# Performance work log

Hardware: AMD Instinct MI355X
Metric: run time of the kernel (lower is better)

The kernel has to match this reference:

```python
import jax, jax.numpy as jnp
import numpy as np

DIM_Q, DIM_K, HEADS = 256, 32, 4
SCALE = (DIM_Q // HEADS) ** (-0.5)


def setup_inputs() -> dict:
    key = jax.random.key(0)
    ks = jax.random.split(key, 12)
    B, C, H, W, D = 2, DIM_Q, 16, 16, 16
    inp = {
        'F_VNet': jax.random.normal(ks[0], (B, C, H, W, D), dtype=jnp.float32),
        'F_Knowledge': jax.random.normal(ks[1], (B, DIM_K, H, W, D), dtype=jnp.float32),
        # torch nn.Linear: y = x @ W.T + b, W: [out, in]
        'Wq': jax.random.normal(ks[2], (DIM_Q, DIM_Q), dtype=jnp.float32) * (DIM_Q ** -0.5),
        'bq': jnp.zeros((DIM_Q,), dtype=jnp.float32),
        'Wk': jax.random.normal(ks[3], (DIM_Q, DIM_K), dtype=jnp.float32) * (DIM_K ** -0.5),
        'bk': jnp.zeros((DIM_Q,), dtype=jnp.float32),
        'Wv': jax.random.normal(ks[4], (DIM_Q, DIM_K), dtype=jnp.float32) * (DIM_K ** -0.5),
        'bv': jnp.zeros((DIM_Q,), dtype=jnp.float32),
        'Wo': jax.random.normal(ks[5], (DIM_Q, DIM_Q), dtype=jnp.float32) * (DIM_Q ** -0.5),
        'bo': jnp.zeros((DIM_Q,), dtype=jnp.float32),
    }
    return inp


def reference(F_VNet, F_Knowledge, Wq, bq, Wk, bk, Wv, bv, Wo, bo):
    B, C, H, W, D = F_VNet.shape
    Ck = F_Knowledge.shape[1]
    # flatten spatial dims to tokens: [B, N, C]
    xq = F_VNet.reshape(B, C, -1).transpose(0, 2, 1)          # [B, Nq, dim_q]
    xk = F_Knowledge.reshape(B, Ck, -1).transpose(0, 2, 1)    # [B, Nk, dim_k]
    Q = xq @ Wq.T + bq                                        # [B, Nq, dim_q]
    K = xk @ Wk.T + bk                                        # [B, Nk, dim_q]
    V = xk @ Wv.T + bv                                        # [B, Nk, dim_q]
    attn = jax.nn.softmax(jnp.einsum('bqc,bkc->bqk', Q, K) * SCALE, axis=-1)
    out = jnp.einsum('bqk,bkc->bqc', attn, V)                 # [B, Nq, dim_q]
    out = out @ Wo.T + bo
    out = out.transpose(0, 2, 1).reshape(B, C, H, W, D)
    return F_VNet + out
```

## Files before the change

### kernel.cpp

```cpp
#include <hip/hip_runtime.h>
#include <hip/hip_bf16.h>
#include <cstdint>
#include <cstddef>

#define N_TOK 4096
#define CQ    256
#define CK    32
#define QK_SCALE 0.18033688011112042f

typedef __attribute__((ext_vector_type(4))) float  f32x4;
typedef __attribute__((ext_vector_type(8))) __bf16 bf16x8;
typedef __attribute__((ext_vector_type(4))) short  s16x4;

__device__ __forceinline__ unsigned short f2bf(float f) {
  union { float f; unsigned u; } x; x.f = f;
  unsigned r = x.u + 0x7FFFu + ((x.u >> 16) & 1u);
  return (unsigned short)(r >> 16);
}

__device__ __forceinline__ f32x4 mfma16(bf16x8 a, bf16x8 b, f32x4 c) {
  return __builtin_amdgcn_mfma_f32_16x16x32_bf16(a, b, c, 0, 0, 0);
}

__device__ __forceinline__ float exp2fast(float x) {
#if __has_builtin(__builtin_amdgcn_exp2f)
  return __builtin_amdgcn_exp2f(x);
#else
  float r; asm("v_exp_f32 %0, %1" : "=v"(r) : "v"(x)); return r;
#endif
}

__device__ __forceinline__ int pos2key(int pos) {
  return ((pos >> 3) << 2) + (pos & 3) + (((pos >> 2) & 1) << 4);
}

__global__ __launch_bounds__(256) void prep_kernel(
    const float* __restrict__ Wq, const float* __restrict__ bq,
    const float* __restrict__ Wk, const float* __restrict__ Wv,
    const float* __restrict__ bv, const float* __restrict__ Wo,
    const float* __restrict__ bo, const float* __restrict__ Fk,
    unsigned short* __restrict__ Aqkt, float* __restrict__ bqk,
    unsigned short* __restrict__ W2bf, float* __restrict__ c2,
    unsigned short* __restrict__ Vpv, unsigned short* __restrict__ XkT)
{
  __shared__ float red[256];
  __shared__ unsigned short trs[128][33];
  const int blk = blockIdx.x, t = threadIdx.x;
  if (blk < 32) {
    const int j = blk;
    float acc = 0.f;
    #pragma unroll 16
    for (int i = 0; i < CQ; i++)
      acc = fmaf(Wq[(size_t)i * CQ + t], Wk[(size_t)i * CK + j], acc);
    Aqkt[(size_t)j * CQ + t] = f2bf(QK_SCALE * acc);
    red[t] = bq[t] * Wk[(size_t)t * CK + j];
    __syncthreads();
    for (int s = 128; s > 0; s >>= 1) {
      if (t < s) red[t] += red[t + s];
      __syncthreads();
    }
    if (t == 0) bqk[j] = QK_SCALE * red[0];
  } else if (blk < 64) {
    const int j = blk - 32;
    float acc = 0.f, acc2 = 0.f;
    #pragma unroll 16
    for (int i = 0; i < CQ; i++) {
      float wo = Wo[(size_t)t * CQ + i];
      acc  = fmaf(wo, Wv[(size_t)i * CK + j], acc);
      acc2 = fmaf(wo, bv[i], acc2);
    }
    W2bf[(size_t)t * CK + j] = f2bf(acc);
    if (j == 0) c2[t] = bo[t] + acc2;
  } else {
    const int blk2 = blk - 64;
    const int b = blk2 >> 5;
    const int t0 = (blk2 & 31) << 7;
    #pragma unroll
    for (int i = 0; i < 4; i++) {
      int flat = (i * 256 + t) << 2;
      int r = flat >> 7, c4 = flat & 127;
      float4 v = *(const float4*)(Fk + ((size_t)(b * CK + r)) * N_TOK + t0 + c4);
      ushort4 u = { f2bf(v.x), f2bf(v.y), f2bf(v.z), f2bf(v.w) };
      trs[c4][r] = u.x; trs[c4+1][r] = u.y; trs[c4+2][r] = u.z; trs[c4+3][r] = u.w;
    }
    __syncthreads();
    {
      const int token = t >> 1, half = t & 1;
      unsigned short tmp[16] __attribute__((aligned(16)));
      #pragma unroll
      for (int k = 0; k < 16; k++) tmp[k] = trs[token][half * 16 + k];
      unsigned short* dst = XkT + ((size_t)(b * N_TOK + t0 + token)) * CK + half * 16;
      ((uint4*)dst)[0] = ((const uint4*)tmp)[0];
      ((uint4*)dst)[1] = ((const uint4*)tmp)[1];
    }
    {
      const int ch32l = t >> 6, d = (t & 63) >> 1, ph = t & 1;
      unsigned short tmp[16] __attribute__((aligned(16)));
      #pragma unroll
      for (int i = 0; i < 16; i++) {
        int pos = ph * 16 + i;
        tmp[i] = trs[ch32l * 32 + pos2key(pos)][d];
      }
      unsigned short* dst = Vpv +
          (((size_t)(b * 128 + (t0 >> 5) + ch32l)) * 32 + d) * 32 + ph * 16;
      ((uint4*)dst)[0] = ((const uint4*)tmp)[0];
      ((uint4*)dst)[1] = ((const uint4*)tmp)[1];
    }
  }
}

__global__ __launch_bounds__(256, 2) void fused_kernel(
    const float* __restrict__ X, const unsigned short* __restrict__ Aqkt,
    const float* __restrict__ bqk, const unsigned short* __restrict__ XkT,
    const unsigned short* __restrict__ Vpv,
    const unsigned short* __restrict__ W2bf, const float* __restrict__ c2,
    float* __restrict__ Y)
{
  __shared__ unsigned short qn[16][40] __attribute__((aligned(16)));
  __shared__ float ml[4][2][16];
  __shared__ float ow[4][16][34];

  const int b  = blockIdx.x >> 8;
  const int t0 = (blockIdx.x & 255) << 4;
  const int t = threadIdx.x, w = t >> 6;
  const int lane = t & 63, c = lane & 15, g = lane >> 4;

  f32x4 qacc[2] = {};
  #pragma unroll
  for (int kk = 0; kk < 8; kk++) {
    const float* xb = X + ((size_t)(b * CQ + kk * 32 + g * 8)) * N_TOK + t0 + c;
    union { unsigned short u[8]; bf16x8 v; } a;
    #pragma unroll
    for (int j = 0; j < 8; j++) a.u[j] = f2bf(xb[(size_t)j * N_TOK]);
    #pragma unroll
    for (int nt = 0; nt < 2; nt++) {
      bf16x8 bB = *(const bf16x8*)(Aqkt + (size_t)(nt * 16 + c) * CQ + kk * 32 + g * 8);
      qacc[nt] = mfma16(a.v, bB, qacc[nt]);
    }
  }
  if (w == 0) {
    #pragma unroll
    for (int nt = 0; nt < 2; nt++) {
      float bj = bqk[nt * 16 + c];
      #pragma unroll
      for (int r = 0; r < 4; r++)
        qn[g * 4 + r][nt * 16 + c] = f2bf(qacc[nt][r] + bj);
    }
  }
  __syncthreads();
  const bf16x8 qf = *(const bf16x8*)&qn[c][g * 8];

  const unsigned short* kb = XkT + ((size_t)(b * N_TOK + w * 1024)) * CK;
  const unsigned short* vp = Vpv + (size_t)b * 128 * 1024;
  float mO = -1e30f, lO = 0.f;
  f32x4 O0 = {}, O1 = {};

  for (int chb = 0; chb < 4; chb++) {
    f32x4 sc[4][4];
    #pragma unroll
    for (int it = 0; it < 4; it++)
      #pragma unroll
      for (int nt = 0; nt < 4; nt++) {
        bf16x8 ak = *(const bf16x8*)(kb +
            (size_t)(chb * 256 + it * 64 + nt * 16 + c) * CK + g * 8);
        f32x4 z = {};
        sc[it][nt] = mfma16(ak, qf, z);
      }

    float mx = -1e30f;
    #pragma unroll
    for (int it = 0; it < 4; it++)
      #pragma unroll
      for (int nt = 0; nt < 4; nt++)
        mx = fmaxf(mx, fmaxf(fmaxf(sc[it][nt][0], sc[it][nt][1]),
                             fmaxf(sc[it][nt][2], sc[it][nt][3])));
    mx = fmaxf(mx, __shfl_xor(mx, 16));
    mx = fmaxf(mx, __shfl_xor(mx, 32));

    float l = 0.f;
    s16x4 pf[4][4];
    #pragma unroll
    for (int it = 0; it < 4; it++)
      #pragma unroll
      for (int nt = 0; nt < 4; nt++) {
        float p0 = exp2fast(sc[it][nt][0] - mx);
        float p1 = exp2fast(sc[it][nt][1] - mx);
        float p2 = exp2fast(sc[it][nt][2] - mx);
        float p3 = exp2fast(sc[it][nt][3] - mx);
        l += (p0 + p1) + (p2 + p3);
        union { __hip_bfloat162 h2[2]; s16x4 v; } pu;
        pu.h2[0] = __float22bfloat162_rn(make_float2(p0, p1));
        pu.h2[1] = __float22bfloat162_rn(make_float2(p2, p3));
        pf[it][nt] = pu.v;
      }
    l += __shfl_xor(l, 16);
    l += __shfl_xor(l, 32);

    f32x4 o0 = {}, o1 = {};
    #pragma unroll
    for (int it = 0; it < 4; it++)
      #pragma unroll
      for (int ntp = 0; ntp < 2; ntp++) {
        const int ch32 = w * 32 + chb * 8 + it * 2 + ntp;
        const unsigned short* base = vp + (size_t)ch32 * 1024;
        union { s16x4 h[2]; bf16x8 v; } bu;
        bu.h[0] = pf[it][ntp * 2];
        bu.h[1] = pf[it][ntp * 2 + 1];
        bf16x8 a0 = *(const bf16x8*)(base + c * 32 + g * 8);
        bf16x8 a1 = *(const bf16x8*)(base + (16 + c) * 32 + g * 8);
        o0 = mfma16(a0, bu.v, o0);
        o1 = mfma16(a1, bu.v, o1);
      }

    float mN = fmaxf(mO, mx);
    float fO = exp2fast(mO - mN), fP = exp2fast(mx - mN);
    lO = lO * fO + l * fP;
    #pragma unroll
    for (int r = 0; r < 4; r++) {
      O0[r] = O0[r] * fO + o0[r] * fP;
      O1[r] = O1[r] * fO + o1[r] * fP;
    }
    mO = mN;
  }

  if (lane < 16) { ml[w][0][c] = mO; ml[w][1][c] = lO; }
  #pragma unroll
  for (int r = 0; r < 4; r++) {
    ow[w][c][g * 4 + r]      = O0[r];
    ow[w][c][16 + g * 4 + r] = O1[r];
  }
  __syncthreads();

  float m4[4], l4[4], mM = -1e30f;
  #pragma unroll
  for (int k = 0; k < 4; k++) {
    m4[k] = ml[k][0][c]; l4[k] = ml[k][1][c];
    mM = fmaxf(mM, m4[k]);
  }
  float f4[4], ls = 0.f;
  #pragma unroll
  for (int k = 0; k < 4; k++) {
    f4[k] = exp2fast(m4[k] - mM);
    ls = fmaf(f4[k], l4[k], ls);
  }
  const float inv = 1.0f / ls;
  union { unsigned short u[8]; bf16x8 v; } wb;
  #pragma unroll
  for (int j = 0; j < 8; j++) {
    float acc = 0.f;
    #pragma unroll
    for (int k = 0; k < 4; k++)
      acc = fmaf(f4[k], ow[k][c][g * 8 + j], acc);
    wb.u[j] = f2bf(acc * inv);
  }

  const int m0 = w * 64;
  f32x4 acc2[4] = {};
  #pragma unroll
  for (int mt = 0; mt < 4; mt++) {
    bf16x8 aW = *(const bf16x8*)(W2bf + (size_t)(m0 + mt * 16 + c) * CK + g * 8);
    acc2[mt] = mfma16(aW, wb.v, acc2[mt]);
  }
  #pragma unroll
  for (int mt = 0; mt < 4; mt++)
    #pragma unroll
    for (int r = 0; r < 4; r++) {
      const int row = m0 + mt * 16 + g * 4 + r;
      size_t idx = ((size_t)(b * CQ + row)) * N_TOK + t0 + c;
      Y[idx] = acc2[mt][r] + c2[row] + X[idx];
    }
}

extern "C" void kernel_launch(void* const* d_in, const int* in_sizes, int n_in,
                              void* d_out, int out_size, void* d_ws, size_t ws_size,
                              hipStream_t stream) {
  const float* F  = (const float*)d_in[0];
  const float* Fk = (const float*)d_in[1];
  const float* Wq = (const float*)d_in[2];
  const float* bq = (const float*)d_in[3];
  const float* Wk = (const float*)d_in[4];
  const float* Wv = (const float*)d_in[6];
  const float* bv = (const float*)d_in[7];
  const float* Wo = (const float*)d_in[8];
  const float* bo = (const float*)d_in[9];
  float* Y = (float*)d_out;
  char* ws = (char*)d_ws;
  unsigned short* XkT   = (unsigned short*)(ws);
  unsigned short* Vpv   = (unsigned short*)(ws + (512u << 10));
  unsigned short* Aqkt  = (unsigned short*)(ws + (2048u << 10));
  unsigned short* W2bf  = (unsigned short*)(ws + (2080u << 10));
  float*          bqk   = (float*)(ws + (2112u << 10));
  float*          c2    = (float*)(ws + (2116u << 10));

  prep_kernel <<<128, 256, 0, stream>>>(Wq, bq, Wk, Wv, bv, Wo, bo, Fk,
                                        Aqkt, bqk, W2bf, c2, Vpv, XkT);
  fused_kernel<<<512, 256, 0, stream>>>(F, Aqkt, bqk, XkT, Vpv, W2bf, c2, Y);
}
```

Baseline: 118.0 us.

## Merge prep and attention kernels into one cooperative launch with grid sync

Prep and fused attention bodies now run inside a single cooperative kernel separated by a grid-wide barrier, with the original two-launch path kept as a fallback if the cooperative launch fails. The goal is to remove the second kernel launch and the gap between the two kernels. The Q projection is also split across all four waves, each doing two K-chunks, then reduced through shared memory instead of every wave computing the full projection redundantly. This costs extra shared memory (qp array) and a grid sync that needs all 512 blocks co-resident at two blocks per CU.

```diff
diff --git a/kernel.cpp b/kernel.cpp
--- a/kernel.cpp
+++ b/kernel.cpp
@@ -1,7 +1,10 @@
 #include <hip/hip_runtime.h>
 #include <hip/hip_bf16.h>
+#include <hip/hip_cooperative_groups.h>
 #include <cstdint>
 #include <cstddef>
+
+namespace cg = cooperative_groups;
 
 #define N_TOK 4096
 #define CQ    256
@@ -34,7 +37,8 @@
   return ((pos >> 3) << 2) + (pos & 3) + (((pos >> 2) & 1) << 4);
 }
 
-__global__ __launch_bounds__(256) void prep_kernel(
+__device__ __forceinline__ void prep_body(
+    int blk, int t,
     const float* __restrict__ Wq, const float* __restrict__ bq,
     const float* __restrict__ Wk, const float* __restrict__ Wv,
     const float* __restrict__ bv, const float* __restrict__ Wo,
@@ -45,7 +49,6 @@
 {
   __shared__ float red[256];
   __shared__ unsigned short trs[128][33];
-  const int blk = blockIdx.x, t = threadIdx.x;
   if (blk < 32) {
     const int j = blk;
     float acc = 0.f;
@@ -71,7 +74,7 @@
     }
     W2bf[(size_t)t * CK + j] = f2bf(acc);
     if (j == 0) c2[t] = bo[t] + acc2;
-  } else {
+  } else if (blk < 128) {
     const int blk2 = blk - 64;
     const int b = blk2 >> 5;
     const int t0 = (blk2 & 31) << 7;
@@ -109,7 +112,8 @@
   }
 }
 
-__global__ __launch_bounds__(256, 2) void fused_kernel(
+__device__ __forceinline__ void fused_body(
+    int blk, int t,
     const float* __restrict__ X, const unsigned short* __restrict__ Aqkt,
     const float* __restrict__ bqk, const unsigned short* __restrict__ XkT,
     const unsigned short* __restrict__ Vpv,
@@ -117,17 +121,19 @@
     float* __restrict__ Y)
 {
   __shared__ unsigned short qn[16][40] __attribute__((aligned(16)));
+  __shared__ float qp[4][16][33];
   __shared__ float ml[4][2][16];
   __shared__ float ow[4][16][34];
 
-  const int b  = blockIdx.x >> 8;
-  const int t0 = (blockIdx.x & 255) << 4;
-  const int t = threadIdx.x, w = t >> 6;
+  const int b  = blk >> 8;
+  const int t0 = (blk & 255) << 4;
+  const int w = t >> 6;
   const int lane = t & 63, c = lane & 15, g = lane >> 4;
 
   f32x4 qacc[2] = {};
   #pragma unroll
-  for (int kk = 0; kk < 8; kk++) {
+  for (int ki = 0; ki < 2; ki++) {
+    const int kk = w * 2 + ki;
     const float* xb = X + ((size_t)(b * CQ + kk * 32 + g * 8)) * N_TOK + t0 + c;
     union { unsigned short u[8]; bf16x8 v; } a;
     #pragma unroll
@@ -138,13 +144,20 @@
       qacc[nt] = mfma16(a.v, bB, qacc[nt]);
     }
   }
-  if (w == 0) {
-    #pragma unroll
-    for (int nt = 0; nt < 2; nt++) {
-      float bj = bqk[nt * 16 + c];
-      #pragma unroll
-      for (int r = 0; r < 4; r++)
-        qn[g * 4 + r][nt * 16 + c] = f2bf(qacc[nt][r] + bj);
+  #pragma unroll
+  for (int nt = 0; nt < 2; nt++)
+    #pragma unroll
+    for (int r = 0; r < 4; r++)
+      qp[w][g * 4 + r][nt * 16 + c] = qacc[nt][r];
+  __syncthreads();
+  {
+    const int tok = t >> 4, d2 = (t & 15) * 2;
+    #pragma unroll
+    for (int dd = 0; dd < 2; dd++) {
+      const int d = d2 + dd;
+      float sv = ((qp[0][tok][d] + qp[1][tok][d]) +
+                  (qp[2][tok][d] + qp[3][tok][d])) + bqk[d];
+      qn[tok][d] = f2bf(sv);
     }
   }
   __syncthreads();
@@ -269,6 +282,46 @@
       size_t idx = ((size_t)(b * CQ + row)) * N_TOK + t0 + c;
       Y[idx] = acc2[mt][r] + c2[row] + X[idx];
     }
+}
+
+__global__ __launch_bounds__(256, 2) void mono_kernel(
+    const float* __restrict__ X, const float* __restrict__ Fk,
+    const float* __restrict__ Wq, const float* __restrict__ bq,
+    const float* __restrict__ Wk, const float* __restrict__ Wv,
+    const float* __restrict__ bv, const float* __restrict__ Wo,
+    const float* __restrict__ bo,
+    unsigned short* __restrict__ XkT, unsigned short* __restrict__ Vpv,
+    unsigned short* __restrict__ Aqkt, unsigned short* __restrict__ W2bf,
+    float* __restrict__ bqk, float* __restrict__ c2,
+    float* __restrict__ Y)
+{
+  prep_body(blockIdx.x, threadIdx.x, Wq, bq, Wk, Wv, bv, Wo, bo, Fk,
+            Aqkt, bqk, W2bf, c2, Vpv, XkT);
+  cg::this_grid().sync();
+  fused_body(blockIdx.x, threadIdx.x, X, Aqkt, bqk, XkT, Vpv, W2bf, c2, Y);
+}
+
+__global__ __launch_bounds__(256) void prep_kernel(
+    const float* __restrict__ Wq, const float* __restrict__ bq,
+    const float* __restrict__ Wk, const float* __restrict__ Wv,
+    const float* __restrict__ bv, const float* __restrict__ Wo,
+    const float* __restrict__ bo, const float* __restrict__ Fk,
+    unsigned short* __restrict__ Aqkt, float* __restrict__ bqk,
+    unsigned short* __restrict__ W2bf, float* __restrict__ c2,
+    unsigned short* __restrict__ Vpv, unsigned short* __restrict__ XkT)
+{
+  prep_body(blockIdx.x, threadIdx.x, Wq, bq, Wk, Wv, bv, Wo, bo, Fk,
+            Aqkt, bqk, W2bf, c2, Vpv, XkT);
+}
+
+__global__ __launch_bounds__(256, 2) void fused_kernel(
+    const float* __restrict__ X, const unsigned short* __restrict__ Aqkt,
+    const float* __restrict__ bqk, const unsigned short* __restrict__ XkT,
+    const unsigned short* __restrict__ Vpv,
+    const unsigned short* __restrict__ W2bf, const float* __restrict__ c2,
+    float* __restrict__ Y)
+{
+  fused_body(blockIdx.x, threadIdx.x, X, Aqkt, bqk, XkT, Vpv, W2bf, c2, Y);
 }
 
 extern "C" void kernel_launch(void* const* d_in, const int* in_sizes, int n_in,
@@ -292,7 +345,17 @@
   float*          bqk   = (float*)(ws + (2112u << 10));
   float*          c2    = (float*)(ws + (2116u << 10));
 
-  prep_kernel <<<128, 256, 0, stream>>>(Wq, bq, Wk, Wv, bv, Wo, bo, Fk,
-                                        Aqkt, bqk, W2bf, c2, Vpv, XkT);
-  fused_kernel<<<512, 256, 0, stream>>>(F, Aqkt, bqk, XkT, Vpv, W2bf, c2, Y);
-}
+  void* args[16] = {
+    (void*)&F, (void*)&Fk, (void*)&Wq, (void*)&bq, (void*)&Wk, (void*)&Wv,
+    (void*)&bv, (void*)&Wo, (void*)&bo, (void*)&XkT, (void*)&Vpv,
+    (void*)&Aqkt, (void*)&W2bf, (void*)&bqk, (void*)&c2, (void*)&Y
+  };
+  hipError_t e = hipLaunchCooperativeKernel((const void*)mono_kernel,
+                                            dim3(512), dim3(256),
+                                            args, 0, stream);
+  if (e != hipSuccess) {
+    prep_kernel <<<128, 256, 0, stream>>>(Wq, bq, Wk, Wv, bv, Wo, bo, Fk,
+                                          Aqkt, bqk, W2bf, c2, Vpv, XkT);
+    fused_kernel<<<512, 256, 0, stream>>>(F, Aqkt, bqk, XkT, Vpv, W2bf, c2, Y);
+  }
+}
```

After: 192.8 us. +63.3%, slower.
